# Kernel optimization log

Hardware: AMD Instinct MI355X
Metric: run time of the kernel (lower is better)

The kernel has to match this reference:

```python
import jax, jax.numpy as jnp
import numpy as np

DIM = 1024
HEADS = 16
HEAD_DIM = DIM // HEADS
SCALE = HEAD_DIM ** -0.5
EPS = 1e-5


def layernorm(x, g, b):
    mu = jnp.mean(x, axis=-1, keepdims=True)
    var = jnp.mean((x - mu) ** 2, axis=-1, keepdims=True)
    return (x - mu) * jax.lax.rsqrt(var + EPS) * g + b


def setup_inputs() -> dict:
    key = jax.random.key(0)
    ks = jax.random.split(key, 12)
    B, N = 2, 2048
    s = DIM ** -0.5
    return {
        "q": jax.random.normal(ks[0], (B, N, DIM), jnp.float32),
        "k": jax.random.normal(ks[1], (B, N, DIM), jnp.float32),
        "v": jax.random.normal(ks[2], (B, N, DIM), jnp.float32),
        "gq": jnp.ones((DIM,), jnp.float32), "bq_ln": jnp.zeros((DIM,), jnp.float32),
        "gk": jnp.ones((DIM,), jnp.float32), "bk_ln": jnp.zeros((DIM,), jnp.float32),
        "gv": jnp.ones((DIM,), jnp.float32), "bv_ln": jnp.zeros((DIM,), jnp.float32),
        "Wq": jax.random.normal(ks[3], (DIM, DIM), jnp.float32) * s,
        "bq": jnp.zeros((DIM,), jnp.float32),
        "Wk": jax.random.normal(ks[4], (DIM, DIM), jnp.float32) * s,
        "bk": jnp.zeros((DIM,), jnp.float32),
        "Wv": jax.random.normal(ks[5], (DIM, DIM), jnp.float32) * s,
        "bv": jnp.zeros((DIM,), jnp.float32),
        "Wp": jax.random.normal(ks[6], (DIM, DIM), jnp.float32) * s,
        "bp": jnp.zeros((DIM,), jnp.float32),
    }


def reference(q, k, v, gq, bq_ln, gk, bk_ln, gv, bv_ln, Wq, bq, Wk, bk, Wv, bv, Wp, bp):
    B, Nq, C = q.shape
    Nk, Nv = k.shape[1], v.shape[1]
    qn = layernorm(q, gq, bq_ln)
    kn = layernorm(k, gk, bk_ln)
    vn = layernorm(v, gv, bv_ln)
    # project and split heads -> [B, H, N, hd]
    qh = (qn @ Wq + bq).reshape(B, Nq, HEADS, HEAD_DIM).transpose(0, 2, 1, 3)
    kh = (kn @ Wk + bk).reshape(B, Nk, HEADS, HEAD_DIM).transpose(0, 2, 1, 3)
    vh = (vn @ Wv + bv).reshape(B, Nv, HEADS, HEAD_DIM).transpose(0, 2, 1, 3)
    attn = jnp.einsum("bhqd,bhkd->bhqk", qh, kh) * SCALE
    attn = jax.nn.softmax(attn, axis=-1)
    out = jnp.einsum("bhqk,bhkd->bhqd", attn, vh)
    out = out.transpose(0, 2, 1, 3).reshape(B, Nq, C)
    out = out @ Wp + bp
    return (out, kh, vh)
```

## Files before the change

### kernel.cpp

```cpp
#include <hip/hip_runtime.h>
#include <cstdint>

#define DIMC 1024
#define NSEQ 2048
#define BATCH 2
#define HEADS 16
#define HD 64
#define MROWS (BATCH * NSEQ)

typedef unsigned short u16;
typedef unsigned int u32;
typedef __attribute__((ext_vector_type(8))) short bf16x8;
typedef __attribute__((ext_vector_type(4))) float f32x4;

#if __has_builtin(__builtin_amdgcn_exp2f)
#define EXP2(x) __builtin_amdgcn_exp2f(x)
#else
#define EXP2(x) exp2f(x)
#endif

__device__ __forceinline__ u16 f2bf(float f) {
  union { float f; u32 u; } v; v.f = f;
  u32 u = v.u;
  return (u16)((u + 0x7fffu + ((u >> 16) & 1u)) >> 16);
}
__device__ __forceinline__ u32 pack_rne(float a, float b) {
  return (u32)f2bf(a) | ((u32)f2bf(b) << 16);
}
__device__ __forceinline__ u32 pack_trunc(float a, float b) {
  union { float f; u32 u; } x, y; x.f = a; y.f = b;
  return (x.u >> 16) | (y.u & 0xffff0000u);
}
__device__ __forceinline__ void gload_lds16(const void* g, void* l) {
  __builtin_amdgcn_global_load_lds((const __attribute__((address_space(1))) void*)g,
                                   (__attribute__((address_space(3))) void*)l, 16, 0, 0);
}

__global__ __launch_bounds__(256)
void prep(const float* __restrict__ q, const float* __restrict__ k,
          const float* __restrict__ v,
          const float* __restrict__ gq, const float* __restrict__ bq,
          const float* __restrict__ gk, const float* __restrict__ bk,
          const float* __restrict__ gv, const float* __restrict__ bv,
          const float* __restrict__ w0, const float* __restrict__ w1,
          const float* __restrict__ w2, const float* __restrict__ w3,
          u16* __restrict__ xn, u16* __restrict__ wtout) {
  __shared__ float tile[64][68];
  int tid = threadIdx.x;
  if (blockIdx.x < 3 * MROWS / 4) {
    int wave = tid >> 6, lane = tid & 63;
    int rowid = blockIdx.x * 4 + wave;
    int tensor = rowid >> 12;
    int r = rowid & 4095;
    const float *src, *g, *b;
    if (tensor == 0)      { src = q; g = gq; b = bq; }
    else if (tensor == 1) { src = k; g = gk; b = bk; }
    else                  { src = v; g = gv; b = bv; }
    src += (size_t)r * DIMC;
    u16* dst = xn + (size_t)tensor * MROWS * DIMC + (size_t)r * DIMC;
    float4 x[4];
    float s = 0.f, s2 = 0.f;
    #pragma unroll
    for (int j = 0; j < 4; ++j) {
      x[j] = ((const float4*)src)[j * 64 + lane];
      s  += x[j].x + x[j].y + x[j].z + x[j].w;
      s2 += x[j].x*x[j].x + x[j].y*x[j].y + x[j].z*x[j].z + x[j].w*x[j].w;
    }
    #pragma unroll
    for (int m = 1; m < 64; m <<= 1) { s += __shfl_xor(s, m); s2 += __shfl_xor(s2, m); }
    float mu  = s * (1.0f / DIMC);
    float var = s2 * (1.0f / DIMC) - mu * mu;
    float inv = rsqrtf(var + 1e-5f);
    #pragma unroll
    for (int j = 0; j < 4; ++j) {
      float4 gg = ((const float4*)g)[j * 64 + lane];
      float4 bb = ((const float4*)b)[j * 64 + lane];
      uint2 o;
      o.x = pack_rne((x[j].x - mu) * inv * gg.x + bb.x, (x[j].y - mu) * inv * gg.y + bb.y);
      o.y = pack_rne((x[j].z - mu) * inv * gg.z + bb.z, (x[j].w - mu) * inv * gg.w + bb.w);
      ((uint2*)dst)[j * 64 + lane] = o;
    }
  } else {
    int blk = blockIdx.x - 3 * MROWS / 4;
    int widx = blk >> 8, t = blk & 255;
    int ti = t >> 4, tj = t & 15;
    const float* W = (widx == 0) ? w0 : (widx == 1) ? w1 : (widx == 2) ? w2 : w3;
    u16* O = wtout + (size_t)widx * DIMC * DIMC;
    int rr = tid >> 4, cc = tid & 15;
    #pragma unroll
    for (int p = 0; p < 4; ++p) {
      int r = p * 16 + rr;
      float4 x = *(const float4*)(&W[(size_t)(ti * 64 + r) * DIMC + tj * 64 + cc * 4]);
      *(float4*)(&tile[r][cc * 4]) = x;
    }
    __syncthreads();
    int c = tid >> 2, r0 = (tid & 3) * 16;
    #pragma unroll
    for (int s = 0; s < 2; ++s) {
      int rb = r0 + s * 8;
      uint4 y;
      y.x = pack_rne(tile[rb + 0][c], tile[rb + 1][c]);
      y.y = pack_rne(tile[rb + 2][c], tile[rb + 3][c]);
      y.z = pack_rne(tile[rb + 4][c], tile[rb + 5][c]);
      y.w = pack_rne(tile[rb + 6][c], tile[rb + 7][c]);
      *(uint4*)(&O[(size_t)(tj * 64 + c) * DIMC + ti * 64 + rb]) = y;
    }
  }
}

__global__ __launch_bounds__(256)
void qkv_gemm(const u16* __restrict__ xn, const u16* __restrict__ wt,
              const float* __restrict__ bq, const float* __restrict__ bk,
              const float* __restrict__ bv,
              float* __restrict__ out, u16* __restrict__ qh,
              u16* __restrict__ khb, u16* __restrict__ vtb) {
  __shared__ u16 smem[128 * 136];
  u16* As0 = smem;
  u16* Bs0 = smem + 4096;
  u16* As1 = smem + 8192;
  u16* Bs1 = smem + 12288;
  u16* Ls = smem;
  const int z = blockIdx.z;
  const u16* A  = xn + (size_t)z * MROWS * DIMC;
  const u16* Bt = wt + (size_t)z * DIMC * DIMC;
  const float* bias = (z == 0) ? bq : (z == 1) ? bk : bv;
  const int bm = blockIdx.x, bn = blockIdx.y;
  const int tid = threadIdx.x;
  const int wave = tid >> 6, lane = tid & 63;
  const int wm = (wave & 1) * 64, wn = (wave >> 1) * 64;
  const int row = lane & 15, quad = lane >> 4;
  const float QSCL = 0.18033688011112042f;
  const int e0 = tid * 8, e1 = 2048 + tid * 8;
  const u16* pa0 = A  + (size_t)(bm * 128 + (e0 >> 5)) * DIMC + (e0 & 31);
  const u16* pa1 = A  + (size_t)(bm * 128 + (e1 >> 5)) * DIMC + (e1 & 31);
  const u16* pb0 = Bt + (size_t)(bn * 128 + (e0 >> 5)) * DIMC + (e0 & 31);
  const u16* pb1 = Bt + (size_t)(bn * 128 + (e1 >> 5)) * DIMC + (e1 & 31);
  f32x4 acc[4][4] = {};
  gload_lds16(pa0, As0 + e0); gload_lds16(pb0, Bs0 + e0);
  gload_lds16(pa1, As0 + e1); gload_lds16(pb1, Bs0 + e1);
  pa0 += 32; pa1 += 32; pb0 += 32; pb1 += 32;
  __syncthreads();
  for (int k0 = 0; k0 < DIMC; k0 += 32) {
    const int cur = (k0 >> 5) & 1;
    u16* Asc = cur ? As1 : As0;
    u16* Bsc = cur ? Bs1 : Bs0;
    if (k0 + 32 < DIMC) {
      u16* Asn = cur ? As0 : As1;
      u16* Bsn = cur ? Bs0 : Bs1;
      gload_lds16(pa0, Asn + e0); gload_lds16(pb0, Bsn + e0);
      gload_lds16(pa1, Asn + e1); gload_lds16(pb1, Bsn + e1);
      pa0 += 32; pa1 += 32; pb0 += 32; pb1 += 32;
    }
    bf16x8 a[4], b[4];
    #pragma unroll
    for (int i = 0; i < 4; ++i)
      a[i] = *(const bf16x8*)(&Asc[(wm + i * 16 + row) * 32 + quad * 8]);
    #pragma unroll
    for (int j = 0; j < 4; ++j)
      b[j] = *(const bf16x8*)(&Bsc[(wn + j * 16 + row) * 32 + quad * 8]);
    #pragma unroll
    for (int i = 0; i < 4; ++i)
      #pragma unroll
      for (int j = 0; j < 4; ++j)
        acc[i][j] = __builtin_amdgcn_mfma_f32_16x16x32_bf16(a[i], b[j], acc[i][j], 0, 0, 0);
    __syncthreads();
  }
  #pragma unroll
  for (int i = 0; i < 4; ++i) {
    #pragma unroll
    for (int j = 0; j < 4; ++j) {
      float val[4];
      #pragma unroll
      for (int r = 0; r < 4; ++r) {
        int m = bm * 128 + wm + i * 16 + quad * 4 + r;
        int c = bn * 128 + wn + j * 16 + row;
        val[r] = acc[i][j][r] + bias[c];
        int b_ = m >> 11, n = m & 2047, h = c >> 6, d = c & 63;
        int bh = b_ * HEADS + h;
        size_t hidx = ((size_t)bh * NSEQ + n) * HD + d;
        if (z == 0) {
          qh[hidx] = f2bf(val[r] * QSCL);
        } else {
          out[(size_t)z * MROWS * DIMC + hidx] = val[r];
          if (z == 1) khb[hidx] = f2bf(val[r]);
        }
      }
      if (z == 2) {
        int ct = wn + j * 16 + row;
        int mt = wm + i * 16 + quad * 4;
        u32* L = (u32*)(&Ls[ct * 136 + mt]);
        L[0] = pack_rne(val[0], val[1]);
        L[1] = pack_rne(val[2], val[3]);
      }
    }
  }
  if (z == 2) {
    __syncthreads();
    int b_ = (bm * 128) >> 11;
    int nbase = (bm * 128) & 2047;
    #pragma unroll
    for (int it = 0; it < 8; ++it) {
      int idx = it * 256 + tid;
      int ct = idx >> 4, ch = idx & 15;
      uint4 y = *(const uint4*)(&Ls[ct * 136 + ch * 8]);
      int c = bn * 128 + ct;
      int h = c >> 6, d = c & 63;
      size_t rowb = ((size_t)(b_ * HEADS + h) * HD + d) * NSEQ;
      int K0 = nbase + ch * 8;
      int d1 = (K0 & ~31) + ((K0 & 8) ? 16 : 0) + ((K0 & 16) ? 4 : 0);
      uint2 lo; lo.x = y.x; lo.y = y.y;
      uint2 hi; hi.x = y.z; hi.y = y.w;
      *(uint2*)(&vtb[rowb + d1])     = lo;
      *(uint2*)(&vtb[rowb + d1 + 8]) = hi;
    }
  }
}

__global__ __launch_bounds__(256)
void out_gemm(const u16* __restrict__ A, const u16* __restrict__ Bt,
              const float* __restrict__ bias, float* __restrict__ outf) {
  __shared__ u16 As[2][64 * 32];
  __shared__ u16 Bs[2][64 * 32];
  const int bm = blockIdx.x, bn = blockIdx.y;
  const int tid = threadIdx.x;
  const int wave = tid >> 6, lane = tid & 63;
  const int wm = (wave & 1) * 32, wn = (wave >> 1) * 32;
  const int row = lane & 15, quad = lane >> 4;
  const int e = tid * 8;
  const u16* pa = A  + (size_t)(bm * 64 + (e >> 5)) * DIMC + (e & 31);
  const u16* pb = Bt + (size_t)(bn * 64 + (e >> 5)) * DIMC + (e & 31);
  f32x4 acc[2][2] = {};
  gload_lds16(pa, &As[0][e]);
  gload_lds16(pb, &Bs[0][e]);
  pa += 32; pb += 32;
  __syncthreads();
  for (int k0 = 0; k0 < DIMC; k0 += 32) {
    const int cur = (k0 >> 5) & 1;
    if (k0 + 32 < DIMC) {
      gload_lds16(pa, &As[cur ^ 1][e]);
      gload_lds16(pb, &Bs[cur ^ 1][e]);
      pa += 32; pb += 32;
    }
    bf16x8 a[2], b[2];
    #pragma unroll
    for (int i = 0; i < 2; ++i)
      a[i] = *(const bf16x8*)(&As[cur][(wm + i * 16 + row) * 32 + quad * 8]);
    #pragma unroll
    for (int j = 0; j < 2; ++j)
      b[j] = *(const bf16x8*)(&Bs[cur][(wn + j * 16 + row) * 32 + quad * 8]);
    #pragma unroll
    for (int i = 0; i < 2; ++i)
      #pragma unroll
      for (int j = 0; j < 2; ++j)
        acc[i][j] = __builtin_amdgcn_mfma_f32_16x16x32_bf16(a[i], b[j], acc[i][j], 0, 0, 0);
    __syncthreads();
  }
  #pragma unroll
  for (int i = 0; i < 2; ++i)
    #pragma unroll
    for (int j = 0; j < 2; ++j)
      #pragma unroll
      for (int r = 0; r < 4; ++r) {
        int m = bm * 64 + wm + i * 16 + quad * 4 + r;
        int c = bn * 64 + wn + j * 16 + row;
        outf[(size_t)m * DIMC + c] = acc[i][j][r] + bias[c];
      }
}

__global__ __launch_bounds__(256)
void attn_fused(const u16* __restrict__ qh, const u16* __restrict__ kh,
                const u16* __restrict__ vt, u16* __restrict__ ao) {
  __shared__ u16 Ks[2][64 * 64];
  __shared__ u16 Vs[2][64 * 64];
  const int flat = blockIdx.x;
  const int bh = (flat & 7) * 4 + ((flat >> 3) & 3);
  const int qtile = flat >> 5;
  const int b = bh >> 4, h = bh & 15;
  const int tid = threadIdx.x;
  const int wave = tid >> 6, lane = tid & 63;
  const int qi = lane & 15, quad = lane >> 4;
  const int sw = qi & 7;
  const size_t base = (size_t)bh * NSEQ * HD;
  bf16x8 qf[2][2];
  #pragma unroll
  for (int qt = 0; qt < 2; ++qt) {
    int qrow = qtile * 128 + wave * 32 + qt * 16 + qi;
    #pragma unroll
    for (int dh = 0; dh < 2; ++dh)
      qf[qt][dh] = *(const bf16x8*)(&qh[base + (size_t)qrow * HD + dh * 32 + quad * 8]);
  }
  const int rk0 = tid >> 3, ck0 = tid & 7;
  const int rk1 = 32 + (tid >> 3);
  const int ko0 = rk0 * HD + ((ck0 ^ (rk0 & 7)) * 8);
  const int ko1 = rk1 * HD + ((ck0 ^ (rk1 & 7)) * 8);
  const int vo0 = rk0 * NSEQ + ((ck0 ^ (rk0 & 7)) * 8);
  const int vo1 = rk1 * NSEQ + ((ck0 ^ (rk1 & 7)) * 8);
  const int ldso = tid * 8;
  const u16* kcur = kh + base;
  const u16* vcur = vt + base;
  gload_lds16(kcur + ko0, &Ks[0][ldso]);
  gload_lds16(kcur + ko1, &Ks[0][2048 + ldso]);
  gload_lds16(vcur + vo0, &Vs[0][ldso]);
  gload_lds16(vcur + vo1, &Vs[0][2048 + ldso]);
  kcur += 64 * HD; vcur += 64;
  __syncthreads();
  float li0 = 0.f, li1 = 0.f;
  f32x4 oacc[2][4] = {};
  for (int t = 0; t < NSEQ / 64; ++t) {
    const int cur = t & 1;
    if (t < NSEQ / 64 - 1) {
      u16* kd = &Ks[cur ^ 1][0];
      u16* vd = &Vs[cur ^ 1][0];
      gload_lds16(kcur + ko0, kd + ldso);
      gload_lds16(kcur + ko1, kd + 2048 + ldso);
      gload_lds16(vcur + vo0, vd + ldso);
      gload_lds16(vcur + vo1, vd + 2048 + ldso);
      kcur += 64 * HD; vcur += 64;
    }
    const u16* Kb = &Ks[cur][0];
    const u16* Vb = &Vs[cur][0];
    #pragma unroll
    for (int kc = 0; kc < 2; ++kc) {
      const u16* kr0 = &Kb[((kc * 2) * 16 + qi) * 64];
      const u16* kr1 = &Kb[((kc * 2 + 1) * 16 + qi) * 64];
      bf16x8 ka0 = *(const bf16x8*)(&kr0[(quad ^ sw) * 8]);
      bf16x8 ka1 = *(const bf16x8*)(&kr0[((4 + quad) ^ sw) * 8]);
      bf16x8 kb0 = *(const bf16x8*)(&kr1[(quad ^ sw) * 8]);
      bf16x8 kb1 = *(const bf16x8*)(&kr1[((4 + quad) ^ sw) * 8]);
      bf16x8 vf[4];
      #pragma unroll
      for (int dt = 0; dt < 4; ++dt)
        vf[dt] = *(const bf16x8*)(&Vb[(dt * 16 + qi) * 64 + ((kc * 4 + quad) ^ sw) * 8]);
      f32x4 s00 = {}, s01 = {}, s10 = {}, s11 = {};
      __builtin_amdgcn_s_setprio(1);
      s00 = __builtin_amdgcn_mfma_f32_16x16x32_bf16(ka0, qf[0][0], s00, 0, 0, 0);
      s00 = __builtin_amdgcn_mfma_f32_16x16x32_bf16(ka1, qf[0][1], s00, 0, 0, 0);
      s01 = __builtin_amdgcn_mfma_f32_16x16x32_bf16(kb0, qf[0][0], s01, 0, 0, 0);
      s01 = __builtin_amdgcn_mfma_f32_16x16x32_bf16(kb1, qf[0][1], s01, 0, 0, 0);
      s10 = __builtin_amdgcn_mfma_f32_16x16x32_bf16(ka0, qf[1][0], s10, 0, 0, 0);
      s10 = __builtin_amdgcn_mfma_f32_16x16x32_bf16(ka1, qf[1][1], s10, 0, 0, 0);
      s11 = __builtin_amdgcn_mfma_f32_16x16x32_bf16(kb0, qf[1][0], s11, 0, 0, 0);
      s11 = __builtin_amdgcn_mfma_f32_16x16x32_bf16(kb1, qf[1][1], s11, 0, 0, 0);
      __builtin_amdgcn_s_setprio(0);
      float a0 = EXP2(s00[0]), a1 = EXP2(s00[1]), a2 = EXP2(s00[2]), a3 = EXP2(s00[3]);
      float a4 = EXP2(s01[0]), a5 = EXP2(s01[1]), a6 = EXP2(s01[2]), a7 = EXP2(s01[3]);
      float b0 = EXP2(s10[0]), b1 = EXP2(s10[1]), b2 = EXP2(s10[2]), b3 = EXP2(s10[3]);
      float b4 = EXP2(s11[0]), b5 = EXP2(s11[1]), b6 = EXP2(s11[2]), b7 = EXP2(s11[3]);
      li0 += ((a0 + a1) + (a2 + a3)) + ((a4 + a5) + (a6 + a7));
      li1 += ((b0 + b1) + (b2 + b3)) + ((b4 + b5) + (b6 + b7));
      union { bf16x8 v; u32 u[4]; } pu0, pu1;
      pu0.u[0] = pack_trunc(a0, a1); pu0.u[1] = pack_trunc(a2, a3);
      pu0.u[2] = pack_trunc(a4, a5); pu0.u[3] = pack_trunc(a6, a7);
      pu1.u[0] = pack_trunc(b0, b1); pu1.u[1] = pack_trunc(b2, b3);
      pu1.u[2] = pack_trunc(b4, b5); pu1.u[3] = pack_trunc(b6, b7);
      __builtin_amdgcn_s_setprio(1);
      #pragma unroll
      for (int dt = 0; dt < 4; ++dt) {
        oacc[0][dt] = __builtin_amdgcn_mfma_f32_16x16x32_bf16(vf[dt], pu0.v, oacc[0][dt], 0, 0, 0);
        oacc[1][dt] = __builtin_amdgcn_mfma_f32_16x16x32_bf16(vf[dt], pu1.v, oacc[1][dt], 0, 0, 0);
      }
      __builtin_amdgcn_s_setprio(0);
    }
    __syncthreads();
  }
  li0 += __shfl_xor(li0, 16); li0 += __shfl_xor(li0, 32);
  li1 += __shfl_xor(li1, 16); li1 += __shfl_xor(li1, 32);
  #pragma unroll
  for (int qt = 0; qt < 2; ++qt) {
    float inv = 1.0f / (qt == 0 ? li0 : li1);
    int token = b * NSEQ + qtile * 128 + wave * 32 + qt * 16 + qi;
    #pragma unroll
    for (int dt = 0; dt < 4; ++dt) {
      int col = h * 64 + dt * 16 + quad * 4;
      *(u32*)(&ao[(size_t)token * DIMC + col]) =
          pack_rne(oacc[qt][dt][0] * inv, oacc[qt][dt][1] * inv);
      *(u32*)(&ao[(size_t)token * DIMC + col + 2]) =
          pack_rne(oacc[qt][dt][2] * inv, oacc[qt][dt][3] * inv);
    }
  }
}

extern "C" void kernel_launch(void* const* d_in, const int* in_sizes, int n_in,
                              void* d_out, int out_size, void* d_ws, size_t ws_size,
                              hipStream_t stream) {
  const float* q    = (const float*)d_in[0];
  const float* k    = (const float*)d_in[1];
  const float* v    = (const float*)d_in[2];
  const float* gq   = (const float*)d_in[3];
  const float* bqln = (const float*)d_in[4];
  const float* gk   = (const float*)d_in[5];
  const float* bkln = (const float*)d_in[6];
  const float* gv   = (const float*)d_in[7];
  const float* bvln = (const float*)d_in[8];
  const float* Wq   = (const float*)d_in[9];
  const float* bq   = (const float*)d_in[10];
  const float* Wk   = (const float*)d_in[11];
  const float* bk   = (const float*)d_in[12];
  const float* Wv   = (const float*)d_in[13];
  const float* bv   = (const float*)d_in[14];
  const float* Wp   = (const float*)d_in[15];
  const float* bp   = (const float*)d_in[16];
  float* out = (float*)d_out;

  char* ws = (char*)d_ws;
  u16* xn  = (u16*)(ws);
  u16* wt  = (u16*)(ws + (size_t)25165824);
  u16* qh  = (u16*)(ws + (size_t)33554432);
  u16* khb = (u16*)(ws + (size_t)41943040);
  u16* ao  = (u16*)(ws + (size_t)50331648);
  u16* vtb = (u16*)d_out;

  const size_t WEL = (size_t)DIMC * DIMC;

  prep<<<3 * MROWS / 4 + 1024, 256, 0, stream>>>(q, k, v, gq, bqln, gk, bkln, gv, bvln,
                                                 Wq, Wk, Wv, Wp, xn, wt);
  qkv_gemm<<<dim3(MROWS / 128, DIMC / 128, 3), 256, 0, stream>>>(
      xn, wt, bq, bk, bv, out, qh, khb, vtb);
  attn_fused<<<dim3((NSEQ / 128) * BATCH * HEADS), 256, 0, stream>>>(qh, khb, vtb, ao);
  out_gemm<<<dim3(MROWS / 64, DIMC / 64), 256, 0, stream>>>(ao, wt + 3 * WEL, bp, out);
}
```

Measured before the change: 251.3 us.

## Split attention key range across two wave groups with LDS reduction

The attention kernel now runs 512 threads per block. Two halves of four waves each process separate halves of the key sequence with their own double-buffered K/V LDS tiles. At the end, the second half writes its partial output accumulators and row sums to LDS, and the first half adds them in and normalizes. This shortens each wave's serial loop and adds intra-block parallelism, at the cost of an LDS reduction, more LDS per block and possibly lower block occupancy. The softmax uses no running max, so the partials add directly.

```diff
diff --git a/kernel.cpp b/kernel.cpp
--- a/kernel.cpp
+++ b/kernel.cpp
@@ -267,58 +267,64 @@
       }
 }
 
-__global__ __launch_bounds__(256)
+__global__ __launch_bounds__(512)
 void attn_fused(const u16* __restrict__ qh, const u16* __restrict__ kh,
                 const u16* __restrict__ vt, u16* __restrict__ ao) {
-  __shared__ u16 Ks[2][64 * 64];
-  __shared__ u16 Vs[2][64 * 64];
+  __shared__ u16 smem[32768];
+  u16* KS = smem;
+  u16* VS = smem + 16384;
   const int flat = blockIdx.x;
   const int bh = (flat & 7) * 4 + ((flat >> 3) & 3);
   const int qtile = flat >> 5;
   const int b = bh >> 4, h = bh & 15;
   const int tid = threadIdx.x;
   const int wave = tid >> 6, lane = tid & 63;
+  const int half = wave >> 2;
+  const int wq = wave & 3;
   const int qi = lane & 15, quad = lane >> 4;
   const int sw = qi & 7;
   const size_t base = (size_t)bh * NSEQ * HD;
   bf16x8 qf[2][2];
   #pragma unroll
   for (int qt = 0; qt < 2; ++qt) {
-    int qrow = qtile * 128 + wave * 32 + qt * 16 + qi;
+    int qrow = qtile * 128 + wq * 32 + qt * 16 + qi;
     #pragma unroll
     for (int dh = 0; dh < 2; ++dh)
       qf[qt][dh] = *(const bf16x8*)(&qh[base + (size_t)qrow * HD + dh * 32 + quad * 8]);
   }
-  const int rk0 = tid >> 3, ck0 = tid & 7;
-  const int rk1 = 32 + (tid >> 3);
+  const int htid = tid & 255;
+  const int rk0 = htid >> 3, ck0 = htid & 7;
+  const int rk1 = 32 + (htid >> 3);
   const int ko0 = rk0 * HD + ((ck0 ^ (rk0 & 7)) * 8);
   const int ko1 = rk1 * HD + ((ck0 ^ (rk1 & 7)) * 8);
   const int vo0 = rk0 * NSEQ + ((ck0 ^ (rk0 & 7)) * 8);
   const int vo1 = rk1 * NSEQ + ((ck0 ^ (rk1 & 7)) * 8);
-  const int ldso = tid * 8;
-  const u16* kcur = kh + base;
-  const u16* vcur = vt + base;
-  gload_lds16(kcur + ko0, &Ks[0][ldso]);
-  gload_lds16(kcur + ko1, &Ks[0][2048 + ldso]);
-  gload_lds16(vcur + vo0, &Vs[0][ldso]);
-  gload_lds16(vcur + vo1, &Vs[0][2048 + ldso]);
+  const int ldso = htid * 8;
+  u16* Kh = KS + half * 8192;
+  u16* Vh = VS + half * 8192;
+  const u16* kcur = kh + base + (size_t)(half * 1024) * HD;
+  const u16* vcur = vt + base + half * 1024;
+  gload_lds16(kcur + ko0, Kh + ldso);
+  gload_lds16(kcur + ko1, Kh + 2048 + ldso);
+  gload_lds16(vcur + vo0, Vh + ldso);
+  gload_lds16(vcur + vo1, Vh + 2048 + ldso);
   kcur += 64 * HD; vcur += 64;
   __syncthreads();
   float li0 = 0.f, li1 = 0.f;
   f32x4 oacc[2][4] = {};
-  for (int t = 0; t < NSEQ / 64; ++t) {
+  for (int t = 0; t < 16; ++t) {
     const int cur = t & 1;
-    if (t < NSEQ / 64 - 1) {
-      u16* kd = &Ks[cur ^ 1][0];
-      u16* vd = &Vs[cur ^ 1][0];
+    if (t < 15) {
+      u16* kd = Kh + (cur ^ 1) * 4096;
+      u16* vd = Vh + (cur ^ 1) * 4096;
       gload_lds16(kcur + ko0, kd + ldso);
       gload_lds16(kcur + ko1, kd + 2048 + ldso);
       gload_lds16(vcur + vo0, vd + ldso);
       gload_lds16(vcur + vo1, vd + 2048 + ldso);
       kcur += 64 * HD; vcur += 64;
     }
-    const u16* Kb = &Ks[cur][0];
-    const u16* Vb = &Vs[cur][0];
+    const u16* Kb = Kh + cur * 4096;
+    const u16* Vb = Vh + cur * 4096;
     #pragma unroll
     for (int kc = 0; kc < 2; ++kc) {
       const u16* kr0 = &Kb[((kc * 2) * 16 + qi) * 64];
@@ -363,19 +369,44 @@
     }
     __syncthreads();
   }
-  li0 += __shfl_xor(li0, 16); li0 += __shfl_xor(li0, 32);
-  li1 += __shfl_xor(li1, 16); li1 += __shfl_xor(li1, 32);
-  #pragma unroll
-  for (int qt = 0; qt < 2; ++qt) {
-    float inv = 1.0f / (qt == 0 ? li0 : li1);
-    int token = b * NSEQ + qtile * 128 + wave * 32 + qt * 16 + qi;
-    #pragma unroll
-    for (int dt = 0; dt < 4; ++dt) {
-      int col = h * 64 + dt * 16 + quad * 4;
-      *(u32*)(&ao[(size_t)token * DIMC + col]) =
-          pack_rne(oacc[qt][dt][0] * inv, oacc[qt][dt][1] * inv);
-      *(u32*)(&ao[(size_t)token * DIMC + col + 2]) =
-          pack_rne(oacc[qt][dt][2] * inv, oacc[qt][dt][3] * inv);
+  float* cb = (float*)smem;
+  const int idx = wq * 64 + lane;
+  if (half == 1) {
+    #pragma unroll
+    for (int qt = 0; qt < 2; ++qt)
+      #pragma unroll
+      for (int dt = 0; dt < 4; ++dt)
+        #pragma unroll
+        for (int r = 0; r < 4; ++r)
+          cb[(qt * 16 + dt * 4 + r) * 256 + idx] = oacc[qt][dt][r];
+    cb[32 * 256 + idx] = li0;
+    cb[33 * 256 + idx] = li1;
+  }
+  __syncthreads();
+  if (half == 0) {
+    #pragma unroll
+    for (int qt = 0; qt < 2; ++qt)
+      #pragma unroll
+      for (int dt = 0; dt < 4; ++dt)
+        #pragma unroll
+        for (int r = 0; r < 4; ++r)
+          oacc[qt][dt][r] += cb[(qt * 16 + dt * 4 + r) * 256 + idx];
+    li0 += cb[32 * 256 + idx];
+    li1 += cb[33 * 256 + idx];
+    li0 += __shfl_xor(li0, 16); li0 += __shfl_xor(li0, 32);
+    li1 += __shfl_xor(li1, 16); li1 += __shfl_xor(li1, 32);
+    #pragma unroll
+    for (int qt = 0; qt < 2; ++qt) {
+      float inv = 1.0f / (qt == 0 ? li0 : li1);
+      int token = b * NSEQ + qtile * 128 + wq * 32 + qt * 16 + qi;
+      #pragma unroll
+      for (int dt = 0; dt < 4; ++dt) {
+        int col = h * 64 + dt * 16 + quad * 4;
+        *(u32*)(&ao[(size_t)token * DIMC + col]) =
+            pack_rne(oacc[qt][dt][0] * inv, oacc[qt][dt][1] * inv);
+        *(u32*)(&ao[(size_t)token * DIMC + col + 2]) =
+            pack_rne(oacc[qt][dt][2] * inv, oacc[qt][dt][3] * inv);
+      }
     }
   }
 }
@@ -416,6 +447,6 @@
                                                  Wq, Wk, Wv, Wp, xn, wt);
   qkv_gemm<<<dim3(MROWS / 128, DIMC / 128, 3), 256, 0, stream>>>(
       xn, wt, bq, bk, bv, out, qh, khb, vtb);
-  attn_fused<<<dim3((NSEQ / 128) * BATCH * HEADS), 256, 0, stream>>>(qh, khb, vtb, ao);
+  attn_fused<<<dim3((NSEQ / 128) * BATCH * HEADS), 512, 0, stream>>>(qh, khb, vtb, ao);
   out_gemm<<<dim3(MROWS / 64, DIMC / 64), 256, 0, stream>>>(ao, wt + 3 * WEL, bp, out);
 }
```

Measured after the change: 243.7 us. -3.0%, faster.
